# Kernel optimization log

Hardware: AMD Instinct MI355X
Metric: run time of the kernel (lower is better)

Reference implementation:

```python
import jax, jax.numpy as jnp
import numpy as np

N = 50000    # num_nodes
E = 800000   # num_edges
IN = 256     # input_dim
H = 256      # hidden_dim
EPS = 1e-5   # BatchNorm eps


def setup_inputs() -> dict:
    key = jax.random.key(0)
    ks = jax.random.split(key, 12)
    def nrm(k, shp, s=0.05):
        return jax.random.normal(k, shp, dtype=jnp.float32) * s
    return {
        "x": jax.random.normal(ks[0], (N, IN), dtype=jnp.float32),
        "edge_index": jax.random.randint(ks[1], (2, E), 0, N, dtype=jnp.int32),
        "edge_weight": jax.random.uniform(ks[2], (E,), dtype=jnp.float32),
        # GCNConv 1 / 2 (PyG stores weight as [in, out]; bias [out])
        "W1": nrm(ks[3], (IN, H)), "b1": jnp.zeros((H,), jnp.float32),
        "W2": nrm(ks[4], (H, H)), "b2": jnp.zeros((H,), jnp.float32),
        # BatchNorm1d 1 / 2
        "gamma1": jnp.ones((H,), jnp.float32), "beta1": jnp.zeros((H,), jnp.float32),
        "gamma2": jnp.ones((H,), jnp.float32), "beta2": jnp.zeros((H,), jnp.float32),
        # LSTM 1 (input 2H) and LSTM 2 (input H), PyTorch gate order i,f,g,o
        "Wih1": nrm(ks[5], (4 * H, 2 * H)), "Whh1": nrm(ks[6], (4 * H, H)),
        "bih1": jnp.zeros((4 * H,), jnp.float32), "bhh1": jnp.zeros((4 * H,), jnp.float32),
        "Wih2": nrm(ks[7], (4 * H, H)), "Whh2": nrm(ks[8], (4 * H, H)),
        "bih2": jnp.zeros((4 * H,), jnp.float32), "bhh2": jnp.zeros((4 * H,), jnp.float32),
    }


def reference(x, edge_index, edge_weight, W1, b1, W2, b2, gamma1, beta1,
              gamma2, beta2, Wih1, Whh1, bih1, bhh1, Wih2, Whh2, bih2, bhh2):
    src, dst = edge_index[0], edge_index[1]
    # GCN symmetric normalization with added self-loops (fill value 1.0)
    loops = jnp.arange(N, dtype=src.dtype)
    src_a = jnp.concatenate([src, loops])
    dst_a = jnp.concatenate([dst, loops])
    ew_a = jnp.concatenate([edge_weight, jnp.ones((N,), edge_weight.dtype)])
    deg = jax.ops.segment_sum(ew_a, dst_a, num_segments=N)
    deg_safe = jnp.where(deg > 0, deg, 1.0)
    dinv = jnp.where(deg > 0, jax.lax.rsqrt(deg_safe), 0.0)
    norm = dinv[src_a] * ew_a * dinv[dst_a]  # [E+N]

    def gcn(h, W, b):
        m = (h @ W)[src_a] * norm[:, None]               # gather + scale messages
        return jax.ops.segment_sum(m, dst_a, num_segments=N) + b

    def bn(h, g, bta):  # training-mode BatchNorm1d (batch stats, biased var)
        mu = jnp.mean(h, axis=0)
        var = jnp.mean((h - mu) ** 2, axis=0)
        return (h - mu) * jax.lax.rsqrt(var + EPS) * g + bta

    def lstm_step0(inp, Wih, bih, bhh):  # single step from h0=c0=0 (window=1)
        gates = inp @ Wih.T + bih + bhh  # Whh term vanishes since h0=0
        i, f, g, o = jnp.split(gates, 4, axis=-1)
        c = jax.nn.sigmoid(i) * jnp.tanh(g)  # f*c0 = 0
        return jax.nn.sigmoid(o) * jnp.tanh(c)

    h1 = bn(jax.nn.relu(gcn(x, W1, b1)), gamma1, beta1)   # [N, H]
    h2 = bn(jax.nn.relu(gcn(h1, W2, b2)), gamma2, beta2)  # [N, H]
    Xc = jnp.concatenate([h1, h2], axis=1)                # [N, 2H]
    hL1 = lstm_step0(Xc, Wih1, bih1, bhh1)                # LSTM1 final hidden
    hL2 = lstm_step0(hL1, Wih2, bih2, bhh2)               # LSTM2 final hidden
    # S with window=1 reduces to x itself
    return jnp.concatenate([hL1, hL2, x], axis=1)         # [N, 2H + IN]
```

## Files before the change

### kernel.cpp

```cpp
#include <hip/hip_runtime.h>
#include <math.h>

#define NN 50000
#define NE 800000

typedef __attribute__((ext_vector_type(8))) short bf8;
typedef __attribute__((ext_vector_type(4))) float f32x4;
typedef unsigned int u32;

__device__ __forceinline__ unsigned short f2b(float f){
  union{float f;unsigned u;} v; v.f=f;
  unsigned r=v.u+0x7fff+((v.u>>16)&1u);
  return (unsigned short)(r>>16);
}
__device__ __forceinline__ float b2f(unsigned short h){
  union{unsigned u;float f;} v; v.u=((unsigned)h)<<16; return v.f;
}
__device__ __forceinline__ float fsigm(float x){ return __builtin_amdgcn_rcpf(1.f+__expf(-x)); }
__device__ __forceinline__ float ftanh(float x){ return 1.f-2.f*__builtin_amdgcn_rcpf(__expf(2.f*x)+1.f); }

__device__ __forceinline__ void gload16(const unsigned short* g, unsigned short* l){
  __builtin_amdgcn_global_load_lds((const __attribute__((address_space(1))) u32*)g,
                                   (__attribute__((address_space(3))) u32*)l,
                                   16,0,0);
}

__global__ __launch_bounds__(256) void k_init(float* deg,int* cnt,float* colsum,float* colsq){
  int i=blockIdx.x*256+threadIdx.x;
  if(i<NN){deg[i]=1.0f;cnt[i]=0;}
  if(i<256){colsum[i]=0.f;colsq[i]=0.f;}
}

__global__ __launch_bounds__(256) void k_deg(const int* __restrict__ ei,const float* __restrict__ ew,
                                             float* deg,int* cnt){
  int e=blockIdx.x*256+threadIdx.x;
  if(e<NE){int d=ei[NE+e];atomicAdd(&deg[d],ew[e]);atomicAdd(&cnt[d],1);}
}

__global__ __launch_bounds__(256) void k_dinv(const float* __restrict__ deg,float* dinv){
  int i=blockIdx.x*256+threadIdx.x;
  if(i<NN){float d=deg[i];dinv[i]=d>0.f?rsqrtf(d):0.f;}
}

__global__ __launch_bounds__(1024) void k_scan(const int* __restrict__ cnt,int* row_ptr,int* cursor){
  __shared__ int s[1024];
  __shared__ int carry;
  int tid=threadIdx.x;
  if(tid==0)carry=0;
  __syncthreads();
  for(int base=0;base<NN;base+=1024){
    int i=base+tid;
    int v=(i<NN)?cnt[i]:0;
    s[tid]=v;__syncthreads();
    for(int off=1;off<1024;off<<=1){
      int t=(tid>=off)?s[tid-off]:0;
      __syncthreads();
      s[tid]+=t;__syncthreads();
    }
    int excl=carry+s[tid]-v;
    if(i<NN){row_ptr[i]=excl;cursor[i]=excl;}
    __syncthreads();
    if(tid==1023)carry+=s[1023];
    __syncthreads();
  }
  if(tid==0)row_ptr[NN]=carry;
}

__global__ __launch_bounds__(256) void k_scatter(const int* __restrict__ ei,const float* __restrict__ ew,
    const float* __restrict__ dinv,int* cursor,int* csr_src,float* csr_w){
  int e=blockIdx.x*256+threadIdx.x;
  if(e<NE){
    int s=ei[e],d=ei[NE+e];
    float wv=dinv[s]*ew[e]*dinv[d];
    int p=atomicAdd(&cursor[d],1);
    csr_src[p]=s;csr_w[p]=wv;
  }
}

__global__ __launch_bounds__(256) void k_wt(const float* __restrict__ W,unsigned short* __restrict__ Wt){
  int j=blockIdx.x,k=threadIdx.x;
  Wt[j*256+k]=f2b(W[k*256+j]);
}
__global__ __launch_bounds__(256) void k_f2b(const float* __restrict__ s,unsigned short* __restrict__ d,int n){
  int i=blockIdx.x*256+threadIdx.x;
  if(i<n)d[i]=f2b(s[i]);
}
__global__ __launch_bounds__(256) void k_cast(const float* __restrict__ s,unsigned short* __restrict__ d){
  long i=(long)blockIdx.x*256+threadIdx.x;
  float4 v=*(const float4*)&s[i*4];
  ushort4 o;o.x=f2b(v.x);o.y=f2b(v.y);o.z=f2b(v.z);o.w=f2b(v.w);
  *(ushort4*)&d[i*4]=o;
}
__global__ __launch_bounds__(256) void k_bsum(const float* __restrict__ a,const float* __restrict__ b,
                                              float* __restrict__ s,int n){
  int i=blockIdx.x*256+threadIdx.x;
  if(i<n)s[i]=a[i]+b[i];
}

__global__ __launch_bounds__(256) void k_foldw(const float* __restrict__ W,
    const float* __restrict__ scale,const float* __restrict__ shift,
    unsigned short* __restrict__ Wt,float* __restrict__ tw){
  __shared__ float red[256];
  int j=blockIdx.x,k=threadIdx.x;
  float w=W[k*256+j];
  Wt[j*256+k]=f2b(w*scale[k]);
  red[k]=w*shift[k];
  __syncthreads();
  for(int off=128;off>0;off>>=1){ if(k<off)red[k]+=red[k+off]; __syncthreads(); }
  if(k==0)tw[j]=red[0];
}

__global__ __launch_bounds__(256) void k_foldlstm(const float* __restrict__ Wih,int K,
    const float* __restrict__ scale,const float* __restrict__ shift,
    const float* __restrict__ bih,const float* __restrict__ bhh,
    unsigned short* __restrict__ Wb,float* __restrict__ bs){
  __shared__ float red[256];
  int m=blockIdx.x,t=threadIdx.x;
  float part=0.f;
  for(int k=t;k<K;k+=256){
    float w=Wih[(long)m*K+k];
    Wb[(long)m*K+k]=f2b(w*scale[k]);
    part+=w*shift[k];
  }
  red[t]=part;
  __syncthreads();
  for(int off=128;off>0;off>>=1){ if(t<off)red[t]+=red[t+off]; __syncthreads(); }
  if(t==0)bs[m]=bih[m]+bhh[m]+red[0];
}

__global__ __launch_bounds__(256,2) void k_gemm_mfma(
    const unsigned short* __restrict__ A,int lda,const unsigned short* __restrict__ Bt,int K,
    unsigned short* __restrict__ Cb){
  __shared__ unsigned short As[2][4096];
  __shared__ unsigned short Bs[2][4096];
  int tid=threadIdx.x;
  int row0=blockIdx.x*128,col0=blockIdx.y*128;
  int lane=tid&63,l15=lane&15,quad=lane>>4;
  int wid=tid>>6,wm=wid>>1,wn=wid&1;
  int sr=tid>>2;
  int aoff=((tid&3)^((tid>>3)&3))*8;
  int xq=quad^((l15>>1)&3);
  long ar0=row0+sr;    if(ar0>=NN)ar0=NN-1;
  long ar1=row0+64+sr; if(ar1>=NN)ar1=NN-1;
  const unsigned short* a0p=A+ar0*lda+aoff;
  const unsigned short* a1p=A+ar1*lda+aoff;
  const unsigned short* b0p=Bt+(long)(col0+sr)*K+aoff;
  const unsigned short* b1p=Bt+(long)(col0+64+sr)*K+aoff;
  int lb=wid*512;
  f32x4 acc[4][4]={};
  int nt=K/32;
  gload16(a0p,&As[0][lb]); gload16(a1p,&As[0][2048+lb]);
  gload16(b0p,&Bs[0][lb]); gload16(b1p,&Bs[0][2048+lb]);
  __syncthreads();
  for(int t=0;t<nt;t++){
    int cur=t&1;
    if(t+1<nt){
      int k0=(t+1)*32;int nxt=cur^1;
      gload16(a0p+k0,&As[nxt][lb]); gload16(a1p+k0,&As[nxt][2048+lb]);
      gload16(b0p+k0,&Bs[nxt][lb]); gload16(b1p+k0,&Bs[nxt][2048+lb]);
    }
    bf8 af[4],bfg[4];
    #pragma unroll
    for(int i=0;i<4;i++){
      af[i] =*(const bf8*)&As[cur][(wm*64+i*16+l15)*32+xq*8];
      bfg[i]=*(const bf8*)&Bs[cur][(wn*64+i*16+l15)*32+xq*8];
    }
    #pragma unroll
    for(int mi=0;mi<4;mi++)
      #pragma unroll
      for(int ni=0;ni<4;ni++)
        acc[mi][ni]=__builtin_amdgcn_mfma_f32_16x16x32_bf16(af[mi],bfg[ni],acc[mi][ni],0,0,0);
    __syncthreads();
  }
  #pragma unroll
  for(int mi=0;mi<4;mi++){
    #pragma unroll
    for(int r=0;r<4;r++){
      int node=row0+wm*64+mi*16+quad*4+r;
      if(node>=NN)continue;
      #pragma unroll
      for(int ni=0;ni<4;ni++){
        int col=col0+wn*64+ni*16+l15;
        Cb[(long)node*256+col]=f2b(acc[mi][ni][r]);
      }
    }
  }
}

__global__ __launch_bounds__(256,2) void k_lstm_mfma(
    const unsigned short* __restrict__ A,int lda,int K,
    const unsigned short* __restrict__ Wb,const float* __restrict__ bsum,
    float* __restrict__ Hout,int ldh,unsigned short* __restrict__ Hb){
  __shared__ unsigned short As[2][4096];
  __shared__ unsigned short Bs[2][6144];
  int tid=threadIdx.x;
  int row0=blockIdx.x*128,m0=blockIdx.y*64;
  int lane=tid&63,l15=lane&15,quad=lane>>4;
  int wid=tid>>6,wm=wid>>1,wn=wid&1;
  int sr=tid>>2;
  int aoff=((tid&3)^((tid>>3)&3))*8;
  int xq=quad^((l15>>1)&3);
  long ar0=row0+sr;    if(ar0>=NN)ar0=NN-1;
  long ar1=row0+64+sr; if(ar1>=NN)ar1=NN-1;
  const unsigned short* a0p=A+ar0*lda+aoff;
  const unsigned short* a1p=A+ar1*lda+aoff;
  const unsigned short* wip=Wb+(long)(    m0+sr)*K+aoff;
  const unsigned short* wgp=Wb+(long)(512+m0+sr)*K+aoff;
  const unsigned short* wop=Wb+(long)(768+m0+sr)*K+aoff;
  int lb=wid*512;
  f32x4 ai[4][2]={},ag[4][2]={},ao[4][2]={};
  int nt=K/32;
  gload16(a0p,&As[0][lb]); gload16(a1p,&As[0][2048+lb]);
  gload16(wip,&Bs[0][lb]); gload16(wgp,&Bs[0][2048+lb]); gload16(wop,&Bs[0][4096+lb]);
  __syncthreads();
  for(int t=0;t<nt;t++){
    int cur=t&1;
    if(t+1<nt){
      int k0=(t+1)*32;int nxt=cur^1;
      gload16(a0p+k0,&As[nxt][lb]); gload16(a1p+k0,&As[nxt][2048+lb]);
      gload16(wip+k0,&Bs[nxt][lb]); gload16(wgp+k0,&Bs[nxt][2048+lb]); gload16(wop+k0,&Bs[nxt][4096+lb]);
    }
    bf8 af[4],bi[2],bg[2],bo[2];
    #pragma unroll
    for(int i=0;i<4;i++)af[i]=*(const bf8*)&As[cur][(wm*64+i*16+l15)*32+xq*8];
    #pragma unroll
    for(int ni=0;ni<2;ni++){
      int rr=wn*32+ni*16+l15;
      bi[ni]=*(const bf8*)&Bs[cur][(    rr)*32+xq*8];
      bg[ni]=*(const bf8*)&Bs[cur][( 64+rr)*32+xq*8];
      bo[ni]=*(const bf8*)&Bs[cur][(128+rr)*32+xq*8];
    }
    #pragma unroll
    for(int mi=0;mi<4;mi++)
      #pragma unroll
      for(int ni=0;ni<2;ni++){
        ai[mi][ni]=__builtin_amdgcn_mfma_f32_16x16x32_bf16(af[mi],bi[ni],ai[mi][ni],0,0,0);
        ag[mi][ni]=__builtin_amdgcn_mfma_f32_16x16x32_bf16(af[mi],bg[ni],ag[mi][ni],0,0,0);
        ao[mi][ni]=__builtin_amdgcn_mfma_f32_16x16x32_bf16(af[mi],bo[ni],ao[mi][ni],0,0,0);
      }
    __syncthreads();
  }
  #pragma unroll
  for(int ni=0;ni<2;ni++){
    int m=m0+wn*32+ni*16+l15;
    float b_i=bsum[m],b_g=bsum[512+m],b_o=bsum[768+m];
    #pragma unroll
    for(int mi=0;mi<4;mi++){
      #pragma unroll
      for(int r=0;r<4;r++){
        int node=row0+wm*64+mi*16+quad*4+r;
        if(node>=NN)continue;
        float gi=ai[mi][ni][r]+b_i;
        float gg=ag[mi][ni][r]+b_g;
        float go=ao[mi][ni][r]+b_o;
        float c=fsigm(gi)*ftanh(gg);
        float h=fsigm(go)*ftanh(c);
        Hout[(long)node*ldh+m]=h;
        if(Hb)Hb[(long)node*256+m]=f2b(h);
      }
    }
  }
}

__global__ __launch_bounds__(256) void k_spmm(const unsigned short* __restrict__ Tb,
    const int* __restrict__ row_ptr,const int* __restrict__ csr_src,const float* __restrict__ csr_w,
    const float* __restrict__ dinv,const float* __restrict__ bias,const float* __restrict__ tw,
    unsigned short* __restrict__ Xb,float* colsum,float* colsq){
  __shared__ float s_sum[4][256];
  __shared__ float s_sq[4][256];
  int tid=threadIdx.x;
  int lane=tid&63,wv=tid>>6;
  int c4=lane*4;
  float4 bc=*(const float4*)&bias[c4];
  float4 twc=make_float4(0.f,0.f,0.f,0.f);
  if(tw)twc=*(const float4*)&tw[c4];
  float sum0=0.f,sum1=0.f,sum2=0.f,sum3=0.f;
  float sq0=0.f,sq1=0.f,sq2=0.f,sq3=0.f;
  int rowbase=blockIdx.x*16+wv*4;
  int rr[4];bool v[4];int p0[4],len[4];
  float acc[4][4];float rs[4];
  int Lmax=0;
  #pragma unroll
  for(int q=0;q<4;q++){
    int r=rowbase+q;
    v[q]=r<NN;
    int rc=v[q]?r:0;
    rr[q]=rc;
    int a=row_ptr[rc],b=row_ptr[rc+1];
    p0[q]=a;len[q]=v[q]?(b-a):0;
    Lmax=max(Lmax,len[q]);
    float di=dinv[rc];float ws=di*di;
    rs[q]=ws;
    ushort4 ts=*(const ushort4*)&Tb[(long)rc*256+c4];
    acc[q][0]=ws*b2f(ts.x);acc[q][1]=ws*b2f(ts.y);acc[q][2]=ws*b2f(ts.z);acc[q][3]=ws*b2f(ts.w);
  }
  for(int j=0;j<Lmax;j++){
    int idx[4];float wq[4];int sidx[4];
    #pragma unroll
    for(int q=0;q<4;q++){
      idx[q]=(j<len[q])?(p0[q]+j):p0[q];
      wq[q]=(j<len[q])?csr_w[idx[q]]:0.f;
      int s=csr_src[idx[q]];sidx[q]=min(max(s,0),NN-1);
    }
    #pragma unroll
    for(int q=0;q<4;q++){
      ushort4 t=*(const ushort4*)&Tb[(long)sidx[q]*256+c4];
      acc[q][0]+=wq[q]*b2f(t.x);acc[q][1]+=wq[q]*b2f(t.y);
      acc[q][2]+=wq[q]*b2f(t.z);acc[q][3]+=wq[q]*b2f(t.w);
      rs[q]+=wq[q];
    }
  }
  #pragma unroll
  for(int q=0;q<4;q++){
    if(!v[q])continue;
    float a0=fmaxf(acc[q][0]+rs[q]*twc.x+bc.x,0.f);
    float a1=fmaxf(acc[q][1]+rs[q]*twc.y+bc.y,0.f);
    float a2=fmaxf(acc[q][2]+rs[q]*twc.z+bc.z,0.f);
    float a3=fmaxf(acc[q][3]+rs[q]*twc.w+bc.w,0.f);
    ushort4 o;o.x=f2b(a0);o.y=f2b(a1);o.z=f2b(a2);o.w=f2b(a3);
    *(ushort4*)&Xb[(long)rr[q]*512+c4]=o;
    sum0+=a0;sum1+=a1;sum2+=a2;sum3+=a3;
    sq0+=a0*a0;sq1+=a1*a1;sq2+=a2*a2;sq3+=a3*a3;
  }
  s_sum[wv][c4+0]=sum0;s_sum[wv][c4+1]=sum1;s_sum[wv][c4+2]=sum2;s_sum[wv][c4+3]=sum3;
  s_sq[wv][c4+0]=sq0;s_sq[wv][c4+1]=sq1;s_sq[wv][c4+2]=sq2;s_sq[wv][c4+3]=sq3;
  __syncthreads();
  if(tid<256){
    float a=s_sum[0][tid]+s_sum[1][tid]+s_sum[2][tid]+s_sum[3][tid];
    float q=s_sq[0][tid]+s_sq[1][tid]+s_sq[2][tid]+s_sq[3][tid];
    atomicAdd(&colsum[tid],a);
    atomicAdd(&colsq[tid],q);
  }
}

__global__ __launch_bounds__(256) void k_bnfin(const float* __restrict__ gamma,const float* __restrict__ beta,
    float* colsum,float* colsq,float* scale,float* shift){
  int c=threadIdx.x;
  float mu=colsum[c]/(float)NN;
  float var=colsq[c]/(float)NN-mu*mu;
  float r=rsqrtf(var+1e-5f);
  float sc=r*gamma[c];
  scale[c]=sc;
  shift[c]=beta[c]-mu*sc;
  colsum[c]=0.f;colsq[c]=0.f;
}

__global__ __launch_bounds__(256) void k_copy_out(const float* __restrict__ src,
    float* __restrict__ out,int colofs){
  long idx=(long)blockIdx.x*256+threadIdx.x;
  long r=idx>>6;int cc=(int)(idx&63)*4;
  if(r<NN)*(float4*)&out[r*768+colofs+cc]=*(const float4*)&src[r*256+cc];
}

extern "C" void kernel_launch(void* const* d_in,const int* in_sizes,int n_in,
                              void* d_out,int out_size,void* d_ws,size_t ws_size,
                              hipStream_t stream){
  const float* x   =(const float*)d_in[0];
  const int*   ei  =(const int*)  d_in[1];
  const float* ew  =(const float*)d_in[2];
  const float* W1  =(const float*)d_in[3];
  const float* b1  =(const float*)d_in[4];
  const float* W2  =(const float*)d_in[5];
  const float* b2  =(const float*)d_in[6];
  const float* g1  =(const float*)d_in[7];
  const float* be1 =(const float*)d_in[8];
  const float* g2  =(const float*)d_in[9];
  const float* be2 =(const float*)d_in[10];
  const float* Wih1=(const float*)d_in[11];
  const float* bih1=(const float*)d_in[13];
  const float* bhh1=(const float*)d_in[14];
  const float* Wih2=(const float*)d_in[15];
  const float* bih2=(const float*)d_in[17];
  const float* bhh2=(const float*)d_in[18];
  float* out=(float*)d_out;

  char* w=(char*)d_ws;
  auto alloc=[&](size_t bytes)->char*{char* p=w;w+=(bytes+255)&~(size_t)255;return p;};
  float* deg    =(float*)alloc((size_t)NN*4);
  float* dinv   =(float*)alloc((size_t)NN*4);
  int*   cnt    =(int*)  alloc((size_t)NN*4);
  int*   row_ptr=(int*)  alloc((size_t)(NN+1)*4);
  int*   cursor =(int*)  alloc((size_t)NN*4);
  int*   csr_src=(int*)  alloc((size_t)NE*4);
  float* csr_w  =(float*)alloc((size_t)NE*4);
  float* colsum =(float*)alloc(256*4);
  float* colsq  =(float*)alloc(256*4);
  float* scale  =(float*)alloc(512*4);
  float* shift  =(float*)alloc(512*4);
  float* tw     =(float*)alloc(256*4);
  unsigned short* Xcb =(unsigned short*)alloc((size_t)NN*512*2);
  unsigned short* TbH =(unsigned short*)alloc((size_t)NN*256*2);
  unsigned short* xb  =(unsigned short*)alloc((size_t)NN*256*2);
  unsigned short* Wt1 =(unsigned short*)alloc(256*256*2);
  unsigned short* Wt2 =(unsigned short*)alloc(256*256*2);
  unsigned short* Wb1 =(unsigned short*)alloc((size_t)1024*512*2);
  unsigned short* Wb2 =(unsigned short*)alloc((size_t)1024*256*2);
  float* bs1 =(float*)alloc(1024*4);
  float* bs2 =(float*)alloc(1024*4);

  int nb=(NN+255)/256;
  k_init<<<nb,256,0,stream>>>(deg,cnt,colsum,colsq);
  k_deg<<<(NE+255)/256,256,0,stream>>>(ei,ew,deg,cnt);
  k_dinv<<<nb,256,0,stream>>>(deg,dinv);
  k_scan<<<1,1024,0,stream>>>(cnt,row_ptr,cursor);
  k_scatter<<<(NE+255)/256,256,0,stream>>>(ei,ew,dinv,cursor,csr_src,csr_w);

  k_wt<<<256,256,0,stream>>>(W1,Wt1);
  k_cast<<<12500,256,0,stream>>>(x,xb);
  k_f2b<<<(1024*256+255)/256,256,0,stream>>>(Wih2,Wb2,1024*256);
  k_bsum<<<4,256,0,stream>>>(bih2,bhh2,bs2,1024);

  int ngx=(NN+127)/128;
  dim3 gd(ngx,2);
  dim3 gl(ngx,4);
  int nspmm=(NN+15)/16;

  k_gemm_mfma<<<gd,256,0,stream>>>(xb,256,Wt1,256,TbH);
  k_spmm<<<nspmm,256,0,stream>>>(TbH,row_ptr,csr_src,csr_w,dinv,b1,nullptr,Xcb+0,colsum,colsq);
  k_bnfin<<<1,256,0,stream>>>(g1,be1,colsum,colsq,scale,shift);
  k_foldw<<<256,256,0,stream>>>(W2,scale,shift,Wt2,tw);
  k_gemm_mfma<<<gd,256,0,stream>>>(Xcb,512,Wt2,256,TbH);
  k_spmm<<<nspmm,256,0,stream>>>(TbH,row_ptr,csr_src,csr_w,dinv,b2,tw,Xcb+256,colsum,colsq);
  k_bnfin<<<1,256,0,stream>>>(g2,be2,colsum,colsq,scale+256,shift+256);
  k_foldlstm<<<1024,256,0,stream>>>(Wih1,512,scale,shift,bih1,bhh1,Wb1,bs1);
  k_lstm_mfma<<<gl,256,0,stream>>>(Xcb,512,512,Wb1,bs1,out+0,768,TbH);
  k_lstm_mfma<<<gl,256,0,stream>>>(TbH,256,256,Wb2,bs2,out+256,768,nullptr);
  k_copy_out<<<12500,256,0,stream>>>(x,out,512);
}
```

Measured before the change: 881.9 us.

## Chunk GEMM output by column for SpMM, parallelize CSR scan, pack edge data

The GEMM now writes its output in a 32-column-chunked layout. The SpMM is reworked so each block handles one 32-column chunk for 16 rows, with 16 lanes per row and an unrolled edge loop, so gathers touch compact 64-byte rows. The single-block serial prefix scan is replaced by a three-kernel multi-block wave-shuffle scan. CSR source and weight are packed into one int2 array read with nontemporal loads. In exchange there are more SpMM blocks, eight times the row_ptr and edge-list reads, and more column-stat atomics.

Result: no change. 884.7 us (+0.3%).

```diff
diff --git a/kernel.cpp b/kernel.cpp
--- a/kernel.cpp
+++ b/kernel.cpp
@@ -7,6 +7,7 @@
 typedef __attribute__((ext_vector_type(8))) short bf8;
 typedef __attribute__((ext_vector_type(4))) float f32x4;
 typedef unsigned int u32;
+typedef unsigned long long u64;
 
 __device__ __forceinline__ unsigned short f2b(float f){
   union{float f;unsigned u;} v; v.f=f;
@@ -16,6 +17,8 @@
 __device__ __forceinline__ float b2f(unsigned short h){
   union{unsigned u;float f;} v; v.u=((unsigned)h)<<16; return v.f;
 }
+__device__ __forceinline__ float lo_bf(u32 t){ union{u32 u;float f;} v; v.u=t<<16; return v.f; }
+__device__ __forceinline__ float hi_bf(u32 t){ union{u32 u;float f;} v; v.u=t&0xffff0000u; return v.f; }
 __device__ __forceinline__ float fsigm(float x){ return __builtin_amdgcn_rcpf(1.f+__expf(-x)); }
 __device__ __forceinline__ float ftanh(float x){ return 1.f-2.f*__builtin_amdgcn_rcpf(__expf(2.f*x)+1.f); }
 
@@ -25,6 +28,12 @@
                                    16,0,0);
 }
 
+__device__ __forceinline__ int wscan_incl(int v,int lane){
+  #pragma unroll
+  for(int d=1;d<64;d<<=1){ int t=__shfl_up(v,d,64); if(lane>=d)v+=t; }
+  return v;
+}
+
 __global__ __launch_bounds__(256) void k_init(float* deg,int* cnt,float* colsum,float* colsq){
   int i=blockIdx.x*256+threadIdx.x;
   if(i<NN){deg[i]=1.0f;cnt[i]=0;}
@@ -42,38 +51,50 @@
   if(i<NN){float d=deg[i];dinv[i]=d>0.f?rsqrtf(d):0.f;}
 }
 
-__global__ __launch_bounds__(1024) void k_scan(const int* __restrict__ cnt,int* row_ptr,int* cursor){
-  __shared__ int s[1024];
-  __shared__ int carry;
+__global__ __launch_bounds__(1024) void k_scan1(const int* __restrict__ cnt,int* row_ptr,int* bsum){
+  __shared__ int wsum[16];
+  __shared__ int woff[17];
+  int tid=threadIdx.x,lane=tid&63,w=tid>>6;
+  int i=blockIdx.x*1024+tid;
+  int v=(i<NN)?cnt[i]:0;
+  int incl=wscan_incl(v,lane);
+  if(lane==63)wsum[w]=incl;
+  __syncthreads();
+  if(w==0){
+    int t=(lane<16)?wsum[lane]:0;
+    int s=wscan_incl(t,lane);
+    if(lane<16)woff[lane+1]=s;
+    if(lane==0)woff[0]=0;
+  }
+  __syncthreads();
+  int excl=incl-v+woff[w];
+  if(i<NN)row_ptr[i]=excl;
+  if(tid==0)bsum[blockIdx.x]=woff[16];
+}
+__global__ __launch_bounds__(64) void k_scan2(int* bsum,int* bbase,int* row_ptr,int nblk){
   int tid=threadIdx.x;
-  if(tid==0)carry=0;
-  __syncthreads();
-  for(int base=0;base<NN;base+=1024){
-    int i=base+tid;
-    int v=(i<NN)?cnt[i]:0;
-    s[tid]=v;__syncthreads();
-    for(int off=1;off<1024;off<<=1){
-      int t=(tid>=off)?s[tid-off]:0;
-      __syncthreads();
-      s[tid]+=t;__syncthreads();
-    }
-    int excl=carry+s[tid]-v;
-    if(i<NN){row_ptr[i]=excl;cursor[i]=excl;}
-    __syncthreads();
-    if(tid==1023)carry+=s[1023];
-    __syncthreads();
-  }
-  if(tid==0)row_ptr[NN]=carry;
+  int v=(tid<nblk)?bsum[tid]:0;
+  int incl=wscan_incl(v,tid);
+  bbase[tid]=incl-v;
+  if(tid==63)row_ptr[NN]=incl;
+}
+__global__ __launch_bounds__(256) void k_scan3(int* row_ptr,int* cursor,const int* __restrict__ bbase){
+  int i=blockIdx.x*256+threadIdx.x;
+  if(i<NN){
+    int r=row_ptr[i]+bbase[i>>10];
+    row_ptr[i]=r;cursor[i]=r;
+  }
 }
 
 __global__ __launch_bounds__(256) void k_scatter(const int* __restrict__ ei,const float* __restrict__ ew,
-    const float* __restrict__ dinv,int* cursor,int* csr_src,float* csr_w){
+    const float* __restrict__ dinv,int* cursor,int2* csr_sw){
   int e=blockIdx.x*256+threadIdx.x;
   if(e<NE){
     int s=ei[e],d=ei[NE+e];
     float wv=dinv[s]*ew[e]*dinv[d];
     int p=atomicAdd(&cursor[d],1);
-    csr_src[p]=s;csr_w[p]=wv;
+    int2 o;o.x=s;o.y=__float_as_int(wv);
+    csr_sw[p]=o;
   }
 }
 
@@ -181,7 +202,7 @@
       #pragma unroll
       for(int ni=0;ni<4;ni++){
         int col=col0+wn*64+ni*16+l15;
-        Cb[(long)node*256+col]=f2b(acc[mi][ni][r]);
+        Cb[((size_t)(col>>5)*NN+node)*32+(col&31)]=f2b(acc[mi][ni][r]);
       }
     }
   }
@@ -262,74 +283,70 @@
   }
 }
 
-__global__ __launch_bounds__(256) void k_spmm(const unsigned short* __restrict__ Tb,
-    const int* __restrict__ row_ptr,const int* __restrict__ csr_src,const float* __restrict__ csr_w,
+__global__ __launch_bounds__(256) void k_spmm8(const unsigned short* __restrict__ T8,
+    const int* __restrict__ row_ptr,const int2* __restrict__ csr_sw,
     const float* __restrict__ dinv,const float* __restrict__ bias,const float* __restrict__ tw,
     unsigned short* __restrict__ Xb,float* colsum,float* colsq){
-  __shared__ float s_sum[4][256];
-  __shared__ float s_sq[4][256];
+  __shared__ float4 s_red[4][16];
   int tid=threadIdx.x;
   int lane=tid&63,wv=tid>>6;
-  int c4=lane*4;
-  float4 bc=*(const float4*)&bias[c4];
-  float4 twc=make_float4(0.f,0.f,0.f,0.f);
-  if(tw)twc=*(const float4*)&tw[c4];
-  float sum0=0.f,sum1=0.f,sum2=0.f,sum3=0.f;
-  float sq0=0.f,sq1=0.f,sq2=0.f,sq3=0.f;
-  int rowbase=blockIdx.x*16+wv*4;
-  int rr[4];bool v[4];int p0[4],len[4];
-  float acc[4][4];float rs[4];
-  int Lmax=0;
+  int g=lane>>4,li=lane&15;
+  int chunk=blockIdx.x&7;
+  int rowblk=blockIdx.x>>3;
+  int r=rowblk*16+wv*4+g;
+  int li2=li*2;
+  int c0=chunk*32+li2;
+  const unsigned short* Tc=T8+(size_t)chunk*NN*32;
+  int p0=row_ptr[r],p1=row_ptr[r+1];
+  int len=p1-p0;
+  float di=dinv[r],ws=di*di;
+  float rs=ws;
+  u32 ts=*(const u32*)&Tc[(size_t)r*32+li2];
+  float acc0=ws*lo_bf(ts),acc1=ws*hi_bf(ts);
+  int Lm=len;
+  Lm=max(Lm,__shfl_xor(Lm,16,64));
+  Lm=max(Lm,__shfl_xor(Lm,32,64));
+  for(int j=0;j<Lm;j+=4){
+    #pragma unroll
+    for(int u=0;u<4;u++){
+      int jj=j+u;
+      bool act=jj<len;
+      int idx=p0+(act?jj:0);
+      idx=min(idx,NE-1);
+      u64 ev=__builtin_nontemporal_load((const u64*)&csr_sw[idx]);
+      int s=(int)(u32)ev;
+      float wgt=act?__int_as_float((int)(ev>>32)):0.f;
+      s=min(max(s,0),NN-1);
+      u32 t=*(const u32*)&Tc[(size_t)s*32+li2];
+      acc0+=wgt*lo_bf(t);
+      acc1+=wgt*hi_bf(t);
+      rs+=wgt;
+    }
+  }
+  float tw0=0.f,tw1=0.f;
+  if(tw){ float2 tc=*(const float2*)&tw[c0]; tw0=tc.x; tw1=tc.y; }
+  float2 bc=*(const float2*)&bias[c0];
+  float a0=fmaxf(acc0+rs*tw0+bc.x,0.f);
+  float a1=fmaxf(acc1+rs*tw1+bc.y,0.f);
+  u32 o=(u32)f2b(a0)|((u32)f2b(a1)<<16);
+  __builtin_nontemporal_store(o,(u32*)&Xb[(size_t)r*512+c0]);
+  float s0=a0,s1=a1,q0=a0*a0,q1=a1*a1;
   #pragma unroll
-  for(int q=0;q<4;q++){
-    int r=rowbase+q;
-    v[q]=r<NN;
-    int rc=v[q]?r:0;
-    rr[q]=rc;
-    int a=row_ptr[rc],b=row_ptr[rc+1];
-    p0[q]=a;len[q]=v[q]?(b-a):0;
-    Lmax=max(Lmax,len[q]);
-    float di=dinv[rc];float ws=di*di;
-    rs[q]=ws;
-    ushort4 ts=*(const ushort4*)&Tb[(long)rc*256+c4];
-    acc[q][0]=ws*b2f(ts.x);acc[q][1]=ws*b2f(ts.y);acc[q][2]=ws*b2f(ts.z);acc[q][3]=ws*b2f(ts.w);
-  }
-  for(int j=0;j<Lmax;j++){
-    int idx[4];float wq[4];int sidx[4];
-    #pragma unroll
-    for(int q=0;q<4;q++){
-      idx[q]=(j<len[q])?(p0[q]+j):p0[q];
-      wq[q]=(j<len[q])?csr_w[idx[q]]:0.f;
-      int s=csr_src[idx[q]];sidx[q]=min(max(s,0),NN-1);
-    }
-    #pragma unroll
-    for(int q=0;q<4;q++){
-      ushort4 t=*(const ushort4*)&Tb[(long)sidx[q]*256+c4];
-      acc[q][0]+=wq[q]*b2f(t.x);acc[q][1]+=wq[q]*b2f(t.y);
-      acc[q][2]+=wq[q]*b2f(t.z);acc[q][3]+=wq[q]*b2f(t.w);
-      rs[q]+=wq[q];
-    }
-  }
-  #pragma unroll
-  for(int q=0;q<4;q++){
-    if(!v[q])continue;
-    float a0=fmaxf(acc[q][0]+rs[q]*twc.x+bc.x,0.f);
-    float a1=fmaxf(acc[q][1]+rs[q]*twc.y+bc.y,0.f);
-    float a2=fmaxf(acc[q][2]+rs[q]*twc.z+bc.z,0.f);
-    float a3=fmaxf(acc[q][3]+rs[q]*twc.w+bc.w,0.f);
-    ushort4 o;o.x=f2b(a0);o.y=f2b(a1);o.z=f2b(a2);o.w=f2b(a3);
-    *(ushort4*)&Xb[(long)rr[q]*512+c4]=o;
-    sum0+=a0;sum1+=a1;sum2+=a2;sum3+=a3;
-    sq0+=a0*a0;sq1+=a1*a1;sq2+=a2*a2;sq3+=a3*a3;
-  }
-  s_sum[wv][c4+0]=sum0;s_sum[wv][c4+1]=sum1;s_sum[wv][c4+2]=sum2;s_sum[wv][c4+3]=sum3;
-  s_sq[wv][c4+0]=sq0;s_sq[wv][c4+1]=sq1;s_sq[wv][c4+2]=sq2;s_sq[wv][c4+3]=sq3;
-  __syncthreads();
-  if(tid<256){
-    float a=s_sum[0][tid]+s_sum[1][tid]+s_sum[2][tid]+s_sum[3][tid];
-    float q=s_sq[0][tid]+s_sq[1][tid]+s_sq[2][tid]+s_sq[3][tid];
-    atomicAdd(&colsum[tid],a);
-    atomicAdd(&colsq[tid],q);
+  for(int m=16;m<=32;m<<=1){
+    s0+=__shfl_xor(s0,m,64); s1+=__shfl_xor(s1,m,64);
+    q0+=__shfl_xor(q0,m,64); q1+=__shfl_xor(q1,m,64);
+  }
+  if(lane<16)s_red[wv][lane]=make_float4(s0,s1,q0,q1);
+  __syncthreads();
+  if(tid<16){
+    float4 a=s_red[0][tid],b=s_red[1][tid],c=s_red[2][tid],d=s_red[3][tid];
+    float f0=a.x+b.x+c.x+d.x;
+    float f1=a.y+b.y+c.y+d.y;
+    float f2=a.z+b.z+c.z+d.z;
+    float f3=a.w+b.w+c.w+d.w;
+    int cc=chunk*32+tid*2;
+    atomicAdd(&colsum[cc],f0);atomicAdd(&colsum[cc+1],f1);
+    atomicAdd(&colsq[cc],f2);atomicAdd(&colsq[cc+1],f3);
   }
 }
 
@@ -381,8 +398,9 @@
   int*   cnt    =(int*)  alloc((size_t)NN*4);
   int*   row_ptr=(int*)  alloc((size_t)(NN+1)*4);
   int*   cursor =(int*)  alloc((size_t)NN*4);
-  int*   csr_src=(int*)  alloc((size_t)NE*4);
-  float* csr_w  =(float*)alloc((size_t)NE*4);
+  int2*  csr_sw =(int2*) alloc((size_t)NE*8);
+  int*   bsum_s =(int*)  alloc(64*4);
+  int*   bbase  =(int*)  alloc(64*4);
   float* colsum =(float*)alloc(256*4);
   float* colsq  =(float*)alloc(256*4);
   float* scale  =(float*)alloc(512*4);
@@ -399,11 +417,14 @@
   float* bs2 =(float*)alloc(1024*4);
 
   int nb=(NN+255)/256;
+  int nsc=(NN+1023)/1024;
   k_init<<<nb,256,0,stream>>>(deg,cnt,colsum,colsq);
   k_deg<<<(NE+255)/256,256,0,stream>>>(ei,ew,deg,cnt);
   k_dinv<<<nb,256,0,stream>>>(deg,dinv);
-  k_scan<<<1,1024,0,stream>>>(cnt,row_ptr,cursor);
-  k_scatter<<<(NE+255)/256,256,0,stream>>>(ei,ew,dinv,cursor,csr_src,csr_w);
+  k_scan1<<<nsc,1024,0,stream>>>(cnt,row_ptr,bsum_s);
+  k_scan2<<<1,64,0,stream>>>(bsum_s,bbase,row_ptr,nsc);
+  k_scan3<<<nb,256,0,stream>>>(row_ptr,cursor,bbase);
+  k_scatter<<<(NE+255)/256,256,0,stream>>>(ei,ew,dinv,cursor,csr_sw);
 
   k_wt<<<256,256,0,stream>>>(W1,Wt1);
   k_cast<<<12500,256,0,stream>>>(x,xb);
@@ -413,14 +434,14 @@
   int ngx=(NN+127)/128;
   dim3 gd(ngx,2);
   dim3 gl(ngx,4);
-  int nspmm=(NN+15)/16;
+  int nspmm=8*(NN/16);
 
   k_gemm_mfma<<<gd,256,0,stream>>>(xb,256,Wt1,256,TbH);
-  k_spmm<<<nspmm,256,0,stream>>>(TbH,row_ptr,csr_src,csr_w,dinv,b1,nullptr,Xcb+0,colsum,colsq);
+  k_spmm8<<<nspmm,256,0,stream>>>(TbH,row_ptr,csr_sw,dinv,b1,nullptr,Xcb+0,colsum,colsq);
   k_bnfin<<<1,256,0,stream>>>(g1,be1,colsum,colsq,scale,shift);
   k_foldw<<<256,256,0,stream>>>(W2,scale,shift,Wt2,tw);
   k_gemm_mfma<<<gd,256,0,stream>>>(Xcb,512,Wt2,256,TbH);
-  k_spmm<<<nspmm,256,0,stream>>>(TbH,row_ptr,csr_src,csr_w,dinv,b2,tw,Xcb+256,colsum,colsq);
+  k_spmm8<<<nspmm,256,0,stream>>>(TbH,row_ptr,csr_sw,dinv,b2,tw,Xcb+256,colsum,colsq);
   k_bnfin<<<1,256,0,stream>>>(g2,be2,colsum,colsq,scale+256,shift+256);
   k_foldlstm<<<1024,256,0,stream>>>(Wih1,512,scale,shift,bih1,bhh1,Wb1,bs1);
   k_lstm_mfma<<<gl,256,0,stream>>>(Xcb,512,512,Wb1,bs1,out+0,768,TbH);
```
